# Performance work log

Measured on AMD Instinct MI355X. Metric: run time of the kernel, lower is better.

Reference implementation:

```python
import jax, jax.numpy as jnp
import numpy as np

W, L, D = 4096, 32, 256
WORD_VOCAB, CHR_VOCAB = 50000, 128


def conv1d(x, w, b):
    # x: [N, C_in, T], w: [C_out, C_in, 3], padding=1 (same)
    y = jax.lax.conv_general_dilated(
        x, w, window_strides=(1,), padding=[(1, 1)],
        dimension_numbers=("NCW", "OIW", "NCW"))
    return y + b[None, :, None]


def setup_inputs() -> dict:
    key = jax.random.key(0)
    ks = jax.random.split(key, 12)
    words = jax.random.randint(ks[0], (W,), 0, WORD_VOCAB, dtype=jnp.int32)
    words_in_char = jax.random.randint(ks[1], (W, L), 0, CHR_VOCAB, dtype=jnp.int32)
    s = 0.02
    word_emb = (jax.random.normal(ks[2], (WORD_VOCAB, D), jnp.float32) * s).at[0].set(0.0)  # padding_idx=0
    chr_emb = (jax.random.normal(ks[3], (CHR_VOCAB, D), jnp.float32) * s).at[0].set(0.0)
    conv_chr_w = jax.random.normal(ks[4], (D, D, 3), jnp.float32) * s
    conv_chr_b = jax.random.normal(ks[5], (D,), jnp.float32) * s
    conv_sent_w = jax.random.normal(ks[6], (2 * D, 2 * D, 3), jnp.float32) * s
    conv_sent_b = jax.random.normal(ks[7], (2 * D,), jnp.float32) * s
    w1 = jax.random.normal(ks[8], (4 * D, 2 * D), jnp.float32) * s
    b1 = jax.random.normal(ks[9], (4 * D,), jnp.float32) * s
    w2 = jax.random.normal(ks[10], (2, 4 * D), jnp.float32) * s
    b2 = jax.random.normal(ks[11], (2,), jnp.float32) * s
    return dict(words=words, words_in_char=words_in_char,
                word_emb=word_emb, chr_emb=chr_emb,
                conv_chr_w=conv_chr_w, conv_chr_b=conv_chr_b,
                conv_sent_w=conv_sent_w, conv_sent_b=conv_sent_b,
                w1=w1, b1=b1, w2=w2, b2=b2)


def reference(words, words_in_char, word_emb, chr_emb,
              conv_chr_w, conv_chr_b, conv_sent_w, conv_sent_b,
              w1, b1, w2, b2):
    # word embeddings: [W, D]
    vector_wrds = word_emb[words]
    # char path, batched over all words (equivalent to the per-word loop):
    ch = chr_emb[words_in_char]                      # [W, L, D]
    ch = jnp.transpose(ch, (0, 2, 1))                # [W, D, L]
    wc = conv1d(ch, conv_chr_w, conv_chr_b)          # [W, D, L]
    vector_wchs = jnp.max(wc, axis=2)                # [W, D]
    # sentence conv over the word axis
    u = jnp.concatenate([vector_wrds, vector_wchs], axis=1)  # [W, 2D]
    u = u.T[None, :, :]                              # [1, 2D, W]
    r = conv1d(u, conv_sent_w, conv_sent_b)          # [1, 2D, W]
    r = jnp.max(r, axis=2)                           # [1, 2D]
    h = jnp.tanh(r @ w1.T + b1)                      # [1, 4D]
    return h @ w2.T + b2                             # [1, 2]
```

## Files before the change

kernel.cpp:

```cpp
#include <hip/hip_runtime.h>
#include <hip/hip_bf16.h>
#include <math.h>

#define NW 4096
#define NL 32
#define ND 256
#define ND2 512

typedef __attribute__((ext_vector_type(8))) short short8;
typedef __attribute__((ext_vector_type(4))) float floatx4;

__device__ inline float bfval(short s) {
  union { unsigned u; float f; } v;
  v.u = ((unsigned)(unsigned short)s) << 16;
  return v.f;
}


__global__ __launch_bounds__(256) void prep_kernel(
    const float* __restrict__ conv_sent_w, const float* __restrict__ conv_chr_w,
    float* __restrict__ wT, __hip_bfloat16* __restrict__ Wb,
    short* __restrict__ u_base) {
  int b = blockIdx.x;
  int tid = threadIdx.x;
  if (b < 3072) {
    int idx = b * 256 + tid;
    float v = conv_sent_w[idx];
    int co = idx / 1536;
    int rem = idx - co * 1536;
    int ci = rem / 3;
    int k = rem - ci * 3;
    Wb[k * 262144 + co * 512 + ci] = __float2bfloat16(v);
  } else if (b < 3840) {
    int idx = (b - 3072) * 256 + tid;
    float v = conv_chr_w[idx];
    int co = idx / 768;
    int rem = idx - co * 768;
    int ci = rem / 3;
    int k = rem - ci * 3;
    wT[k * 65536 + ci * 256 + co] = v;
  } else {
    u_base[tid] = 0;
    u_base[tid + 256] = 0;
    u_base[4097 * 512 + tid] = 0;
    u_base[4097 * 512 + tid + 256] = 0;
  }
}

__global__ __launch_bounds__(256) void table_kernel(
    const float* __restrict__ chr_emb, const float* __restrict__ wT,
    __hip_bfloat16* __restrict__ Tb) {
  __shared__ float s_e[4][256];
  int k = blockIdx.x >> 5;
  int c0 = (blockIdx.x & 31) * 4;
  int co = threadIdx.x;
#pragma unroll
  for (int j = 0; j < 4; ++j) s_e[j][co] = chr_emb[(c0 + j) * 256 + co];
  __syncthreads();
  const float* wk = wT + k * 65536;
  float a0 = 0.f, a1 = 0.f, a2 = 0.f, a3 = 0.f;
#pragma unroll 8
  for (int ci = 0; ci < 256; ++ci) {
    float w = wk[ci * 256 + co];
    a0 = fmaf(s_e[0][ci], w, a0);
    a1 = fmaf(s_e[1][ci], w, a1);
    a2 = fmaf(s_e[2][ci], w, a2);
    a3 = fmaf(s_e[3][ci], w, a3);
  }
  int base = ((co >> 6) * 3 + k) * 8192 + (co & 63);
  Tb[base + (c0 + 0) * 64] = __float2bfloat16(a0);
  Tb[base + (c0 + 1) * 64] = __float2bfloat16(a1);
  Tb[base + (c0 + 2) * 64] = __float2bfloat16(a2);
  Tb[base + (c0 + 3) * 64] = __float2bfloat16(a3);
}

__global__ __launch_bounds__(256) void char_word_kernel(
    const int* __restrict__ words, const int* __restrict__ wic,
    const __hip_bfloat16* __restrict__ Tb, const float* __restrict__ word_emb,
    const float* __restrict__ bias, __hip_bfloat16* __restrict__ u0) {
  __shared__ short sT[3 * 128 * 64];
  __shared__ int s_wic[64 * 32];
  __shared__ int s_wid[64];
  int ct = blockIdx.x >> 6;
  int w0 = (blockIdx.x & 63) * 64;
  int tid = threadIdx.x;
  {
    const uint4* src = (const uint4*)((const short*)Tb + ct * 24576);
    uint4* dst = (uint4*)sT;
#pragma unroll
    for (int i = 0; i < 12; ++i) dst[tid + i * 256] = src[tid + i * 256];
    const int4* wsrc = (const int4*)(wic + w0 * 32);
    int4* wdst = (int4*)s_wic;
    wdst[tid] = wsrc[tid];
    wdst[tid + 256] = wsrc[tid + 256];
    if (tid < 64) s_wid[tid] = words[w0 + tid];
  }
  __syncthreads();
  int co_l = tid & 63;
  int slot = tid >> 6;
  float bb = bias[ct * 64 + co_l];
  const short* T0 = sT;
  const short* T1 = sT + 8192;
  const short* T2 = sT + 16384;
  for (int wi = 0; wi < 16; ++wi) {
    int wl = slot * 16 + wi;
    u0[(w0 + wl) * ND2 + ct * 64 + co_l] =
        __float2bfloat16(word_emb[s_wid[wl] * ND + ct * 64 + co_l]);
    const int* ch = s_wic + wl * 32;
    float m = -INFINITY;
#pragma unroll
    for (int t = 0; t < NL; ++t) {
      float s = bfval(T1[ch[t] * 64 + co_l]);
      if (t > 0) s += bfval(T0[ch[t - 1] * 64 + co_l]);
      if (t < NL - 1) s += bfval(T2[ch[t + 1] * 64 + co_l]);
      m = fmaxf(m, s);
    }
    u0[(w0 + wl) * ND2 + ND + ct * 64 + co_l] = __float2bfloat16(m + bb);
  }
}

__global__ __launch_bounds__(256, 2) void sent_conv_mfma(
    const __hip_bfloat16* __restrict__ u0,
    const __hip_bfloat16* __restrict__ Wb,
    float* __restrict__ partial) {
  __shared__ short As[64 * 64];
  __shared__ short Bs[64 * 64];
  __shared__ float sm[4][32];
  const int tid = threadIdx.x;
  const int t0 = blockIdx.x * 64;
  const int co0 = blockIdx.y * 64;
  const int wave = tid >> 6, lane = tid & 63;
  const int wy = wave >> 1, wx = wave & 1;
  const int m = lane & 15, q = lane >> 4;

  floatx4 acc[2][2];
#pragma unroll
  for (int i = 0; i < 2; ++i)
#pragma unroll
    for (int j = 0; j < 2; ++j) acc[i][j] = (floatx4){0.f, 0.f, 0.f, 0.f};

  int aoff[2][2], boff[2][2];
#pragma unroll
  for (int kk = 0; kk < 2; ++kk) {
#pragma unroll
    for (int i = 0; i < 2; ++i) {
      int row = wy * 32 + i * 16 + m;
      aoff[kk][i] = row * 64 + (((kk * 4 + q) ^ (row & 7)) * 8);
      row = wx * 32 + i * 16 + m;
      boff[kk][i] = row * 64 + (((kk * 4 + q) ^ (row & 7)) * 8);
    }
  }

  const int sc = tid & 7, sr = tid >> 3;
  const int swc = (sc ^ (sr & 7)) * 8;
  const short* WbS = (const short*)Wb;
  const short* uS = (const short*)u0;

  for (int s = 0; s < 24; ++s) {
    int k = s >> 3, ci0 = (s & 7) << 6;
    const short* WbK = WbS + k * 262144 + (co0 + sr) * 512 + ci0 + sc * 8;
    const short* uK = uS + (t0 + sr + k - 1) * 512 + ci0 + sc * 8;
    uint4 a0 = *(const uint4*)(WbK);
    uint4 a1 = *(const uint4*)(WbK + 32 * 512);
    uint4 b0 = *(const uint4*)(uK);
    uint4 b1 = *(const uint4*)(uK + 32 * 512);
    *(uint4*)&As[sr * 64 + swc] = a0;
    *(uint4*)&As[(sr + 32) * 64 + swc] = a1;
    *(uint4*)&Bs[sr * 64 + swc] = b0;
    *(uint4*)&Bs[(sr + 32) * 64 + swc] = b1;
    __syncthreads();
#pragma unroll
    for (int kk = 0; kk < 2; ++kk) {
      short8 av0 = *(const short8*)&As[aoff[kk][0]];
      short8 av1 = *(const short8*)&As[aoff[kk][1]];
      short8 bv0 = *(const short8*)&Bs[boff[kk][0]];
      short8 bv1 = *(const short8*)&Bs[boff[kk][1]];
      acc[0][0] = __builtin_amdgcn_mfma_f32_16x16x32_bf16(av0, bv0, acc[0][0], 0, 0, 0);
      acc[0][1] = __builtin_amdgcn_mfma_f32_16x16x32_bf16(av0, bv1, acc[0][1], 0, 0, 0);
      acc[1][0] = __builtin_amdgcn_mfma_f32_16x16x32_bf16(av1, bv0, acc[1][0], 0, 0, 0);
      acc[1][1] = __builtin_amdgcn_mfma_f32_16x16x32_bf16(av1, bv1, acc[1][1], 0, 0, 0);
    }
    __syncthreads();
  }

#pragma unroll
  for (int i = 0; i < 2; ++i)
#pragma unroll
    for (int r = 0; r < 4; ++r) {
      float x = fmaxf(acc[i][0][r], acc[i][1][r]);
#pragma unroll
      for (int off = 1; off < 16; off <<= 1)
        x = fmaxf(x, __shfl_xor(x, off, 64));
      if (m == 0) sm[wave][i * 16 + q * 4 + r] = x;
    }
  __syncthreads();
  if (tid < 64) {
    int whalf = tid >> 5;
    float v = fmaxf(sm[whalf * 2 + 0][tid & 31], sm[whalf * 2 + 1][tid & 31]);
    partial[(co0 + tid) * 64 + blockIdx.x] = v;
  }
}

__global__ __launch_bounds__(512) void fc1_kernel(
    const float* __restrict__ partial, const float* __restrict__ bs,
    const float* __restrict__ w1, const float* __restrict__ b1,
    float* __restrict__ h) {
  __shared__ float s_r[512];
  int tid = threadIdx.x;
  {
    const float4* p = (const float4*)(partial + tid * 64);
    float mm = -INFINITY;
#pragma unroll
    for (int j = 0; j < 16; ++j) {
      float4 v = p[j];
      mm = fmaxf(mm, fmaxf(fmaxf(v.x, v.y), fmaxf(v.z, v.w)));
    }
    s_r[tid] = mm + bs[tid];
  }
  __syncthreads();
  int wave = tid >> 6, lane = tid & 63;
  int o = blockIdx.x * 8 + wave;
  const float4* wv = (const float4*)(w1 + o * 512 + lane * 8);
  const float4* rv = (const float4*)(s_r + lane * 8);
  float4 w0 = wv[0], w1v = wv[1];
  float4 r0 = rv[0], r1 = rv[1];
  float acc = w0.x * r0.x + w0.y * r0.y + w0.z * r0.z + w0.w * r0.w +
              w1v.x * r1.x + w1v.y * r1.y + w1v.z * r1.z + w1v.w * r1.w;
#pragma unroll
  for (int off = 32; off >= 1; off >>= 1) acc += __shfl_down(acc, off, 64);
  if (lane == 0) h[o] = tanhf(acc + b1[o]);
}

__global__ __launch_bounds__(128) void fc2_kernel(
    const float* __restrict__ h, const float* __restrict__ w2,
    const float* __restrict__ b2, float* __restrict__ out) {
  int tid = threadIdx.x;
  int o = tid >> 6;
  int lane = tid & 63;
  float acc = 0.f;
#pragma unroll
  for (int j = 0; j < 16; ++j)
    acc = fmaf(w2[o * 1024 + lane + j * 64], h[lane + j * 64], acc);
#pragma unroll
  for (int off = 32; off >= 1; off >>= 1) acc += __shfl_down(acc, off, 64);
  if (lane == 0) out[o] = acc + b2[o];
}

extern "C" void kernel_launch(void* const* d_in, const int* in_sizes, int n_in,
                              void* d_out, int out_size, void* d_ws, size_t ws_size,
                              hipStream_t stream) {
  const int*   words       = (const int*)d_in[0];
  const int*   wic         = (const int*)d_in[1];
  const float* word_emb    = (const float*)d_in[2];
  const float* chr_emb     = (const float*)d_in[3];
  const float* conv_chr_w  = (const float*)d_in[4];
  const float* conv_chr_b  = (const float*)d_in[5];
  const float* conv_sent_w = (const float*)d_in[6];
  const float* conv_sent_b = (const float*)d_in[7];
  const float* w1          = (const float*)d_in[8];
  const float* b1          = (const float*)d_in[9];
  const float* w2          = (const float*)d_in[10];
  const float* b2          = (const float*)d_in[11];
  float* out = (float*)d_out;

  float* ws    = (float*)d_ws;
  float* wT    = ws;
  float* part  = wT + 196608;
  float* h_buf = part + 32768;
  short* Tb    = (short*)(h_buf + 1024);
  short* u_base = Tb + 98304;
  __hip_bfloat16* u0 = (__hip_bfloat16*)(u_base + 512);
  __hip_bfloat16* Wb = (__hip_bfloat16*)(u_base + 4098 * 512);

  prep_kernel<<<3841, 256, 0, stream>>>(conv_sent_w, conv_chr_w, wT, Wb, u_base);
  table_kernel<<<96, 256, 0, stream>>>(chr_emb, wT, (__hip_bfloat16*)Tb);
  char_word_kernel<<<256, 256, 0, stream>>>(words, wic, (const __hip_bfloat16*)Tb,
                                            word_emb, conv_chr_b, u0);
  sent_conv_mfma<<<dim3(64, 8), 256, 0, stream>>>(u0, Wb, part);
  fc1_kernel<<<128, 512, 0, stream>>>(part, conv_sent_b, w1, b1, h_buf);
  fc2_kernel<<<1, 128, 0, stream>>>(h_buf, w2, b2, out);
}
```

Before: 160.1 us.

## Fuse all stages into one persistent kernel with atomic grid barriers

Replaces six launches with a single 256-block persistent kernel whose stages are separated by software grid barriers built on an atomic counter. The char table build now reads conv_chr_w directly through a shared-memory tile instead of a transposed intermediate. The sentence conv tile grows to 128 time steps per block and software-prefetches the next K slice into registers. This removes launch gaps and the wT round trip, but relies on all 256 blocks being co-resident and adds barrier spin costs plus a memset per call.

New measurement: 241.3 us. 50.7% more time.

```diff
diff --git a/kernel.cpp b/kernel.cpp
--- a/kernel.cpp
+++ b/kernel.cpp
@@ -17,233 +17,266 @@
 }
 
 
-__global__ __launch_bounds__(256) void prep_kernel(
-    const float* __restrict__ conv_sent_w, const float* __restrict__ conv_chr_w,
-    float* __restrict__ wT, __hip_bfloat16* __restrict__ Wb,
-    short* __restrict__ u_base) {
-  int b = blockIdx.x;
-  int tid = threadIdx.x;
-  if (b < 3072) {
-    int idx = b * 256 + tid;
-    float v = conv_sent_w[idx];
-    int co = idx / 1536;
-    int rem = idx - co * 1536;
-    int ci = rem / 3;
-    int k = rem - ci * 3;
-    Wb[k * 262144 + co * 512 + ci] = __float2bfloat16(v);
-  } else if (b < 3840) {
-    int idx = (b - 3072) * 256 + tid;
-    float v = conv_chr_w[idx];
-    int co = idx / 768;
-    int rem = idx - co * 768;
-    int ci = rem / 3;
-    int k = rem - ci * 3;
-    wT[k * 65536 + ci * 256 + co] = v;
+union SMem {
+  struct { float w[256][49]; float e[2][256]; } tab;
+  struct { short T[3 * 128 * 64]; int wic[64 * 32]; int wid[64]; } chr;
+  struct { short As[64 * 64]; short Bs[128 * 64]; float red[4][32]; } sent;
+  struct { float r[512]; } fc;
+};
+
+__device__ __forceinline__ void gbar(int* ctr, int expect) {
+  __syncthreads();
+  if (threadIdx.x == 0) {
+    __hip_atomic_fetch_add(ctr, 1, __ATOMIC_RELEASE, __HIP_MEMORY_SCOPE_AGENT);
+    while (__hip_atomic_load(ctr, __ATOMIC_RELAXED, __HIP_MEMORY_SCOPE_AGENT) < expect)
+      __builtin_amdgcn_s_sleep(8);
+    __builtin_amdgcn_fence(__ATOMIC_ACQUIRE, "agent");
+  }
+  __syncthreads();
+}
+
+__global__ __launch_bounds__(256) void fused_kernel(
+    const int* __restrict__ words, const int* __restrict__ wic,
+    const float* __restrict__ word_emb, const float* __restrict__ chr_emb,
+    const float* __restrict__ conv_chr_w, const float* __restrict__ conv_chr_b,
+    const float* __restrict__ conv_sent_w, const float* __restrict__ conv_sent_b,
+    const float* __restrict__ w1, const float* __restrict__ b1,
+    const float* __restrict__ w2, const float* __restrict__ b2,
+    int* __restrict__ ctr, float* __restrict__ part, float* __restrict__ h_buf,
+    short* __restrict__ Tb, short* __restrict__ u_base,
+    __hip_bfloat16* __restrict__ Wb, float* __restrict__ out) {
+  __shared__ SMem S;
+  const int b = blockIdx.x;
+  const int tid = threadIdx.x;
+
+  if (b >= 64) {
+    int base = (b - 64) * 4096;
+#pragma unroll
+    for (int i = 0; i < 16; ++i) {
+      int idx = base + i * 256 + tid;
+      float v = conv_sent_w[idx];
+      int co = idx / 1536;
+      int rem = idx - co * 1536;
+      int ci = rem / 3;
+      int k = rem - ci * 3;
+      Wb[k * 262144 + co * 512 + ci] = __float2bfloat16(v);
+    }
+    if (b == 255) {
+      u_base[tid] = 0; u_base[tid + 256] = 0;
+      u_base[4097 * 512 + tid] = 0; u_base[4097 * 512 + tid + 256] = 0;
+    }
   } else {
-    u_base[tid] = 0;
-    u_base[tid + 256] = 0;
-    u_base[4097 * 512 + tid] = 0;
-    u_base[4097 * 512 + tid + 256] = 0;
-  }
-}
-
-__global__ __launch_bounds__(256) void table_kernel(
-    const float* __restrict__ chr_emb, const float* __restrict__ wT,
-    __hip_bfloat16* __restrict__ Tb) {
-  __shared__ float s_e[4][256];
-  int k = blockIdx.x >> 5;
-  int c0 = (blockIdx.x & 31) * 4;
-  int co = threadIdx.x;
-#pragma unroll
-  for (int j = 0; j < 4; ++j) s_e[j][co] = chr_emb[(c0 + j) * 256 + co];
-  __syncthreads();
-  const float* wk = wT + k * 65536;
-  float a0 = 0.f, a1 = 0.f, a2 = 0.f, a3 = 0.f;
+    const int c0 = b * 2;
+    const int co = tid;
+    S.tab.e[0][tid] = chr_emb[(c0 + 0) * 256 + tid];
+    S.tab.e[1][tid] = chr_emb[(c0 + 1) * 256 + tid];
+    float acc[2][3] = {};
+    for (int chk = 0; chk < 16; ++chk) {
+      const int ci0 = chk * 16;
+      __syncthreads();
 #pragma unroll 8
-  for (int ci = 0; ci < 256; ++ci) {
-    float w = wk[ci * 256 + co];
-    a0 = fmaf(s_e[0][ci], w, a0);
-    a1 = fmaf(s_e[1][ci], w, a1);
-    a2 = fmaf(s_e[2][ci], w, a2);
-    a3 = fmaf(s_e[3][ci], w, a3);
-  }
-  int base = ((co >> 6) * 3 + k) * 8192 + (co & 63);
-  Tb[base + (c0 + 0) * 64] = __float2bfloat16(a0);
-  Tb[base + (c0 + 1) * 64] = __float2bfloat16(a1);
-  Tb[base + (c0 + 2) * 64] = __float2bfloat16(a2);
-  Tb[base + (c0 + 3) * 64] = __float2bfloat16(a3);
-}
-
-__global__ __launch_bounds__(256) void char_word_kernel(
-    const int* __restrict__ words, const int* __restrict__ wic,
-    const __hip_bfloat16* __restrict__ Tb, const float* __restrict__ word_emb,
-    const float* __restrict__ bias, __hip_bfloat16* __restrict__ u0) {
-  __shared__ short sT[3 * 128 * 64];
-  __shared__ int s_wic[64 * 32];
-  __shared__ int s_wid[64];
-  int ct = blockIdx.x >> 6;
-  int w0 = (blockIdx.x & 63) * 64;
-  int tid = threadIdx.x;
+      for (int i = 0; i < 48; ++i) {
+        int f = tid + i * 256;
+        int wco = f / 48;
+        int j = f - wco * 48;
+        S.tab.w[wco][j] = conv_chr_w[wco * 768 + ci0 * 3 + j];
+      }
+      __syncthreads();
+#pragma unroll
+      for (int ci = 0; ci < 16; ++ci) {
+        float t_w0 = S.tab.w[co][ci * 3 + 0];
+        float t_w1 = S.tab.w[co][ci * 3 + 1];
+        float t_w2 = S.tab.w[co][ci * 3 + 2];
+        float e0 = S.tab.e[0][ci0 + ci];
+        float e1 = S.tab.e[1][ci0 + ci];
+        acc[0][0] = fmaf(e0, t_w0, acc[0][0]);
+        acc[0][1] = fmaf(e0, t_w1, acc[0][1]);
+        acc[0][2] = fmaf(e0, t_w2, acc[0][2]);
+        acc[1][0] = fmaf(e1, t_w0, acc[1][0]);
+        acc[1][1] = fmaf(e1, t_w1, acc[1][1]);
+        acc[1][2] = fmaf(e1, t_w2, acc[1][2]);
+      }
+    }
+    __hip_bfloat16* TbB = (__hip_bfloat16*)Tb;
+    const int tbase = ((co >> 6) * 3) * 8192 + (co & 63);
+#pragma unroll
+    for (int k = 0; k < 3; ++k) {
+      TbB[tbase + k * 8192 + (c0 + 0) * 64] = __float2bfloat16(acc[0][k]);
+      TbB[tbase + k * 8192 + (c0 + 1) * 64] = __float2bfloat16(acc[1][k]);
+    }
+  }
+  gbar(ctr, 256);
+
   {
-    const uint4* src = (const uint4*)((const short*)Tb + ct * 24576);
-    uint4* dst = (uint4*)sT;
+    const int ct = b >> 6;
+    const int w0c = (b & 63) * 64;
+    const uint4* src = (const uint4*)(Tb + ct * 24576);
+    uint4* dst = (uint4*)S.chr.T;
 #pragma unroll
     for (int i = 0; i < 12; ++i) dst[tid + i * 256] = src[tid + i * 256];
-    const int4* wsrc = (const int4*)(wic + w0 * 32);
-    int4* wdst = (int4*)s_wic;
+    const int4* wsrc = (const int4*)(wic + w0c * 32);
+    int4* wdst = (int4*)S.chr.wic;
     wdst[tid] = wsrc[tid];
     wdst[tid + 256] = wsrc[tid + 256];
-    if (tid < 64) s_wid[tid] = words[w0 + tid];
-  }
-  __syncthreads();
-  int co_l = tid & 63;
-  int slot = tid >> 6;
-  float bb = bias[ct * 64 + co_l];
-  const short* T0 = sT;
-  const short* T1 = sT + 8192;
-  const short* T2 = sT + 16384;
-  for (int wi = 0; wi < 16; ++wi) {
-    int wl = slot * 16 + wi;
-    u0[(w0 + wl) * ND2 + ct * 64 + co_l] =
-        __float2bfloat16(word_emb[s_wid[wl] * ND + ct * 64 + co_l]);
-    const int* ch = s_wic + wl * 32;
-    float m = -INFINITY;
-#pragma unroll
-    for (int t = 0; t < NL; ++t) {
-      float s = bfval(T1[ch[t] * 64 + co_l]);
-      if (t > 0) s += bfval(T0[ch[t - 1] * 64 + co_l]);
-      if (t < NL - 1) s += bfval(T2[ch[t + 1] * 64 + co_l]);
-      m = fmaxf(m, s);
-    }
-    u0[(w0 + wl) * ND2 + ND + ct * 64 + co_l] = __float2bfloat16(m + bb);
-  }
-}
-
-__global__ __launch_bounds__(256, 2) void sent_conv_mfma(
-    const __hip_bfloat16* __restrict__ u0,
-    const __hip_bfloat16* __restrict__ Wb,
-    float* __restrict__ partial) {
-  __shared__ short As[64 * 64];
-  __shared__ short Bs[64 * 64];
-  __shared__ float sm[4][32];
-  const int tid = threadIdx.x;
-  const int t0 = blockIdx.x * 64;
-  const int co0 = blockIdx.y * 64;
-  const int wave = tid >> 6, lane = tid & 63;
-  const int wy = wave >> 1, wx = wave & 1;
-  const int m = lane & 15, q = lane >> 4;
-
-  floatx4 acc[2][2];
-#pragma unroll
-  for (int i = 0; i < 2; ++i)
-#pragma unroll
-    for (int j = 0; j < 2; ++j) acc[i][j] = (floatx4){0.f, 0.f, 0.f, 0.f};
-
-  int aoff[2][2], boff[2][2];
-#pragma unroll
-  for (int kk = 0; kk < 2; ++kk) {
-#pragma unroll
-    for (int i = 0; i < 2; ++i) {
-      int row = wy * 32 + i * 16 + m;
-      aoff[kk][i] = row * 64 + (((kk * 4 + q) ^ (row & 7)) * 8);
-      row = wx * 32 + i * 16 + m;
-      boff[kk][i] = row * 64 + (((kk * 4 + q) ^ (row & 7)) * 8);
-    }
-  }
-
-  const int sc = tid & 7, sr = tid >> 3;
-  const int swc = (sc ^ (sr & 7)) * 8;
-  const short* WbS = (const short*)Wb;
-  const short* uS = (const short*)u0;
-
-  for (int s = 0; s < 24; ++s) {
-    int k = s >> 3, ci0 = (s & 7) << 6;
-    const short* WbK = WbS + k * 262144 + (co0 + sr) * 512 + ci0 + sc * 8;
-    const short* uK = uS + (t0 + sr + k - 1) * 512 + ci0 + sc * 8;
-    uint4 a0 = *(const uint4*)(WbK);
-    uint4 a1 = *(const uint4*)(WbK + 32 * 512);
-    uint4 b0 = *(const uint4*)(uK);
-    uint4 b1 = *(const uint4*)(uK + 32 * 512);
-    *(uint4*)&As[sr * 64 + swc] = a0;
-    *(uint4*)&As[(sr + 32) * 64 + swc] = a1;
-    *(uint4*)&Bs[sr * 64 + swc] = b0;
-    *(uint4*)&Bs[(sr + 32) * 64 + swc] = b1;
+    if (tid < 64) S.chr.wid[tid] = words[w0c + tid];
     __syncthreads();
+    const int co_l = tid & 63;
+    const int slot = tid >> 6;
+    const float bb = conv_chr_b[ct * 64 + co_l];
+    const short* T0p = S.chr.T;
+    const short* T1p = S.chr.T + 8192;
+    const short* T2p = S.chr.T + 16384;
+    __hip_bfloat16* u0 = (__hip_bfloat16*)(u_base + 512);
+    for (int wi = 0; wi < 16; ++wi) {
+      int wl = slot * 16 + wi;
+      u0[(w0c + wl) * ND2 + ct * 64 + co_l] =
+          __float2bfloat16(word_emb[S.chr.wid[wl] * ND + ct * 64 + co_l]);
+      const int* ch = S.chr.wic + wl * 32;
+      float mx = -INFINITY;
+#pragma unroll
+      for (int t = 0; t < NL; ++t) {
+        float sv = bfval(T1p[ch[t] * 64 + co_l]);
+        if (t > 0) sv += bfval(T0p[ch[t - 1] * 64 + co_l]);
+        if (t < NL - 1) sv += bfval(T2p[ch[t + 1] * 64 + co_l]);
+        mx = fmaxf(mx, sv);
+      }
+      u0[(w0c + wl) * ND2 + ND + ct * 64 + co_l] = __float2bfloat16(mx + bb);
+    }
+  }
+  gbar(ctr, 512);
+
+  {
+    const int co0 = (b & 7) * 64;
+    const int T0 = (b >> 3) * 128;
+    const int wave = tid >> 6, lane = tid & 63;
+    const int wy = wave >> 1, wx = wave & 1;
+    const int m = lane & 15, q = lane >> 4;
+    floatx4 acc[2][4];
+#pragma unroll
+    for (int i = 0; i < 2; ++i)
+#pragma unroll
+      for (int j = 0; j < 4; ++j) acc[i][j] = (floatx4){0.f, 0.f, 0.f, 0.f};
+
+    int aoff[2][2], boff[2][4];
 #pragma unroll
     for (int kk = 0; kk < 2; ++kk) {
-      short8 av0 = *(const short8*)&As[aoff[kk][0]];
-      short8 av1 = *(const short8*)&As[aoff[kk][1]];
-      short8 bv0 = *(const short8*)&Bs[boff[kk][0]];
-      short8 bv1 = *(const short8*)&Bs[boff[kk][1]];
-      acc[0][0] = __builtin_amdgcn_mfma_f32_16x16x32_bf16(av0, bv0, acc[0][0], 0, 0, 0);
-      acc[0][1] = __builtin_amdgcn_mfma_f32_16x16x32_bf16(av0, bv1, acc[0][1], 0, 0, 0);
-      acc[1][0] = __builtin_amdgcn_mfma_f32_16x16x32_bf16(av1, bv0, acc[1][0], 0, 0, 0);
-      acc[1][1] = __builtin_amdgcn_mfma_f32_16x16x32_bf16(av1, bv1, acc[1][1], 0, 0, 0);
-    }
+#pragma unroll
+      for (int i = 0; i < 2; ++i) {
+        int row = wy * 32 + i * 16 + m;
+        aoff[kk][i] = row * 64 + (((kk * 4 + q) ^ (row & 7)) * 8);
+      }
+#pragma unroll
+      for (int j = 0; j < 4; ++j) {
+        int row = (j >> 1) * 64 + wx * 32 + (j & 1) * 16 + m;
+        boff[kk][j] = row * 64 + (((kk * 4 + q) ^ (row & 7)) * 8);
+      }
+    }
+    const int sc = tid & 7, sr = tid >> 3;
+    const int swc = (sc ^ (sr & 7)) * 8;
+    const short* WbS = (const short*)Wb;
+    const short* uS = u_base + 512;
+
+    uint4 ra0, ra1, rb0, rb1, rb2, rb3;
+    auto LOADS = [&](int s2) {
+      int k = s2 >> 3, ci0 = (s2 & 7) << 6;
+      const short* WbK = WbS + k * 262144 + (co0 + sr) * 512 + ci0 + sc * 8;
+      const short* uK = uS + (T0 + sr + k - 1) * 512 + ci0 + sc * 8;
+      ra0 = *(const uint4*)(WbK);
+      ra1 = *(const uint4*)(WbK + 32 * 512);
+      rb0 = *(const uint4*)(uK);
+      rb1 = *(const uint4*)(uK + 32 * 512);
+      rb2 = *(const uint4*)(uK + 64 * 512);
+      rb3 = *(const uint4*)(uK + 96 * 512);
+    };
+    LOADS(0);
+    for (int s = 0; s < 24; ++s) {
+      *(uint4*)&S.sent.As[sr * 64 + swc] = ra0;
+      *(uint4*)&S.sent.As[(sr + 32) * 64 + swc] = ra1;
+      *(uint4*)&S.sent.Bs[sr * 64 + swc] = rb0;
+      *(uint4*)&S.sent.Bs[(sr + 32) * 64 + swc] = rb1;
+      *(uint4*)&S.sent.Bs[(sr + 64) * 64 + swc] = rb2;
+      *(uint4*)&S.sent.Bs[(sr + 96) * 64 + swc] = rb3;
+      __syncthreads();
+      if (s < 23) LOADS(s + 1);
+#pragma unroll
+      for (int kk = 0; kk < 2; ++kk) {
+        short8 av0 = *(const short8*)&S.sent.As[aoff[kk][0]];
+        short8 av1 = *(const short8*)&S.sent.As[aoff[kk][1]];
+        short8 bv0 = *(const short8*)&S.sent.Bs[boff[kk][0]];
+        short8 bv1 = *(const short8*)&S.sent.Bs[boff[kk][1]];
+        short8 bv2 = *(const short8*)&S.sent.Bs[boff[kk][2]];
+        short8 bv3 = *(const short8*)&S.sent.Bs[boff[kk][3]];
+        acc[0][0] = __builtin_amdgcn_mfma_f32_16x16x32_bf16(av0, bv0, acc[0][0], 0, 0, 0);
+        acc[0][1] = __builtin_amdgcn_mfma_f32_16x16x32_bf16(av0, bv1, acc[0][1], 0, 0, 0);
+        acc[0][2] = __builtin_amdgcn_mfma_f32_16x16x32_bf16(av0, bv2, acc[0][2], 0, 0, 0);
+        acc[0][3] = __builtin_amdgcn_mfma_f32_16x16x32_bf16(av0, bv3, acc[0][3], 0, 0, 0);
+        acc[1][0] = __builtin_amdgcn_mfma_f32_16x16x32_bf16(av1, bv0, acc[1][0], 0, 0, 0);
+        acc[1][1] = __builtin_amdgcn_mfma_f32_16x16x32_bf16(av1, bv1, acc[1][1], 0, 0, 0);
+        acc[1][2] = __builtin_amdgcn_mfma_f32_16x16x32_bf16(av1, bv2, acc[1][2], 0, 0, 0);
+        acc[1][3] = __builtin_amdgcn_mfma_f32_16x16x32_bf16(av1, bv3, acc[1][3], 0, 0, 0);
+      }
+      __syncthreads();
+    }
+#pragma unroll
+    for (int i = 0; i < 2; ++i)
+#pragma unroll
+      for (int r = 0; r < 4; ++r) {
+        float x = fmaxf(fmaxf(acc[i][0][r], acc[i][1][r]),
+                        fmaxf(acc[i][2][r], acc[i][3][r]));
+#pragma unroll
+        for (int off = 1; off < 16; off <<= 1)
+          x = fmaxf(x, __shfl_xor(x, off, 64));
+        if (m == 0) S.sent.red[wave][i * 16 + q * 4 + r] = x;
+      }
     __syncthreads();
-  }
-
-#pragma unroll
-  for (int i = 0; i < 2; ++i)
-#pragma unroll
-    for (int r = 0; r < 4; ++r) {
-      float x = fmaxf(acc[i][0][r], acc[i][1][r]);
-#pragma unroll
-      for (int off = 1; off < 16; off <<= 1)
-        x = fmaxf(x, __shfl_xor(x, off, 64));
-      if (m == 0) sm[wave][i * 16 + q * 4 + r] = x;
-    }
-  __syncthreads();
-  if (tid < 64) {
-    int whalf = tid >> 5;
-    float v = fmaxf(sm[whalf * 2 + 0][tid & 31], sm[whalf * 2 + 1][tid & 31]);
-    partial[(co0 + tid) * 64 + blockIdx.x] = v;
-  }
-}
-
-__global__ __launch_bounds__(512) void fc1_kernel(
-    const float* __restrict__ partial, const float* __restrict__ bs,
-    const float* __restrict__ w1, const float* __restrict__ b1,
-    float* __restrict__ h) {
-  __shared__ float s_r[512];
-  int tid = threadIdx.x;
+    if (tid < 64) {
+      int whalf = tid >> 5;
+      float v = fmaxf(S.sent.red[whalf * 2 + 0][tid & 31],
+                      S.sent.red[whalf * 2 + 1][tid & 31]);
+      part[(co0 + tid) * 32 + (b >> 3)] = v;
+    }
+  }
+  gbar(ctr, 768);
+
   {
-    const float4* p = (const float4*)(partial + tid * 64);
-    float mm = -INFINITY;
-#pragma unroll
-    for (int j = 0; j < 16; ++j) {
-      float4 v = p[j];
-      mm = fmaxf(mm, fmaxf(fmaxf(v.x, v.y), fmaxf(v.z, v.w)));
-    }
-    s_r[tid] = mm + bs[tid];
-  }
-  __syncthreads();
-  int wave = tid >> 6, lane = tid & 63;
-  int o = blockIdx.x * 8 + wave;
-  const float4* wv = (const float4*)(w1 + o * 512 + lane * 8);
-  const float4* rv = (const float4*)(s_r + lane * 8);
-  float4 w0 = wv[0], w1v = wv[1];
-  float4 r0 = rv[0], r1 = rv[1];
-  float acc = w0.x * r0.x + w0.y * r0.y + w0.z * r0.z + w0.w * r0.w +
-              w1v.x * r1.x + w1v.y * r1.y + w1v.z * r1.z + w1v.w * r1.w;
-#pragma unroll
-  for (int off = 32; off >= 1; off >>= 1) acc += __shfl_down(acc, off, 64);
-  if (lane == 0) h[o] = tanhf(acc + b1[o]);
-}
-
-__global__ __launch_bounds__(128) void fc2_kernel(
-    const float* __restrict__ h, const float* __restrict__ w2,
-    const float* __restrict__ b2, float* __restrict__ out) {
-  int tid = threadIdx.x;
-  int o = tid >> 6;
-  int lane = tid & 63;
-  float acc = 0.f;
-#pragma unroll
-  for (int j = 0; j < 16; ++j)
-    acc = fmaf(w2[o * 1024 + lane + j * 64], h[lane + j * 64], acc);
-#pragma unroll
-  for (int off = 32; off >= 1; off >>= 1) acc += __shfl_down(acc, off, 64);
-  if (lane == 0) out[o] = acc + b2[o];
+#pragma unroll
+    for (int rep = 0; rep < 2; ++rep) {
+      int row = tid + rep * 256;
+      const float4* p = (const float4*)(part + row * 32);
+      float mm = -INFINITY;
+#pragma unroll
+      for (int j = 0; j < 8; ++j) {
+        float4 v = p[j];
+        mm = fmaxf(mm, fmaxf(fmaxf(v.x, v.y), fmaxf(v.z, v.w)));
+      }
+      S.fc.r[row] = mm + conv_sent_b[row];
+    }
+    __syncthreads();
+    const int wave = tid >> 6, lane = tid & 63;
+    const int o = b * 4 + wave;
+    const float4* wv = (const float4*)(w1 + o * 512 + lane * 8);
+    const float4* rv = (const float4*)(S.fc.r + lane * 8);
+    float4 wv0 = wv[0], wv1 = wv[1];
+    float4 rv0 = rv[0], rv1 = rv[1];
+    float acc = wv0.x * rv0.x + wv0.y * rv0.y + wv0.z * rv0.z + wv0.w * rv0.w +
+                wv1.x * rv1.x + wv1.y * rv1.y + wv1.z * rv1.z + wv1.w * rv1.w;
+#pragma unroll
+    for (int off = 32; off >= 1; off >>= 1) acc += __shfl_down(acc, off, 64);
+    if (lane == 0) h_buf[o] = tanhf(acc + b1[o]);
+  }
+  gbar(ctr, 1024);
+
+  if (b == 0 && tid < 128) {
+    const int o = tid >> 6;
+    const int lane = tid & 63;
+    float acc2 = 0.f;
+#pragma unroll
+    for (int j = 0; j < 16; ++j)
+      acc2 = fmaf(w2[o * 1024 + lane + j * 64], h_buf[lane + j * 64], acc2);
+#pragma unroll
+    for (int off = 32; off >= 1; off >>= 1) acc2 += __shfl_down(acc2, off, 64);
+    if (lane == 0) out[o] = acc2 + b2[o];
+  }
 }
 
 extern "C" void kernel_launch(void* const* d_in, const int* in_sizes, int n_in,
@@ -264,19 +297,15 @@
   float* out = (float*)d_out;
 
   float* ws    = (float*)d_ws;
-  float* wT    = ws;
-  float* part  = wT + 196608;
-  float* h_buf = part + 32768;
+  int*   ctr   = (int*)ws;
+  float* part  = ws + 4;
+  float* h_buf = part + 16384;
   short* Tb    = (short*)(h_buf + 1024);
   short* u_base = Tb + 98304;
-  __hip_bfloat16* u0 = (__hip_bfloat16*)(u_base + 512);
   __hip_bfloat16* Wb = (__hip_bfloat16*)(u_base + 4098 * 512);
 
-  prep_kernel<<<3841, 256, 0, stream>>>(conv_sent_w, conv_chr_w, wT, Wb, u_base);
-  table_kernel<<<96, 256, 0, stream>>>(chr_emb, wT, (__hip_bfloat16*)Tb);
-  char_word_kernel<<<256, 256, 0, stream>>>(words, wic, (const __hip_bfloat16*)Tb,
-                                            word_emb, conv_chr_b, u0);
-  sent_conv_mfma<<<dim3(64, 8), 256, 0, stream>>>(u0, Wb, part);
-  fc1_kernel<<<128, 512, 0, stream>>>(part, conv_sent_b, w1, b1, h_buf);
-  fc2_kernel<<<1, 128, 0, stream>>>(h_buf, w2, b2, out);
+  hipMemsetAsync(ctr, 0, 16, stream);
+  fused_kernel<<<256, 256, 0, stream>>>(words, wic, word_emb, chr_emb,
+      conv_chr_w, conv_chr_b, conv_sent_w, conv_sent_b, w1, b1, w2, b2,
+      ctr, part, h_buf, Tb, u_base, Wb, out);
 }
```

## Fuse char-weight transpose into table kernel and vectorize char conv gather

Applied to the files above, without the earlier changes.

Merges the prep and table kernels so the char conv table is computed directly from conv_chr_w, staged through shared memory. This removes one launch and the intermediate transposed weight buffer. The char_word kernel now runs twice as many blocks, each handling 32 words, and each lane reads packed bf16 pairs with characters preloaded into registers. The goals are higher occupancy, fewer LDS reads and one less kernel boundary. In exchange, the table part now uses only 64 blocks with a long serial loop, and the larger register array may raise register pressure.

After: 184.7 us. +15.4%, slower.

```diff
diff --git a/kernel.cpp b/kernel.cpp
--- a/kernel.cpp
+++ b/kernel.cpp
@@ -10,68 +10,73 @@
 typedef __attribute__((ext_vector_type(8))) short short8;
 typedef __attribute__((ext_vector_type(4))) float floatx4;
 
-__device__ inline float bfval(short s) {
+__device__ inline float bitsf(unsigned u) {
   union { unsigned u; float f; } v;
-  v.u = ((unsigned)(unsigned short)s) << 16;
+  v.u = u;
   return v.f;
 }
 
 
-__global__ __launch_bounds__(256) void prep_kernel(
+__global__ __launch_bounds__(256) void prep_table_kernel(
     const float* __restrict__ conv_sent_w, const float* __restrict__ conv_chr_w,
-    float* __restrict__ wT, __hip_bfloat16* __restrict__ Wb,
-    short* __restrict__ u_base) {
-  int b = blockIdx.x;
-  int tid = threadIdx.x;
-  if (b < 3072) {
-    int idx = b * 256 + tid;
-    float v = conv_sent_w[idx];
-    int co = idx / 1536;
-    int rem = idx - co * 1536;
-    int ci = rem / 3;
-    int k = rem - ci * 3;
-    Wb[k * 262144 + co * 512 + ci] = __float2bfloat16(v);
-  } else if (b < 3840) {
-    int idx = (b - 3072) * 256 + tid;
-    float v = conv_chr_w[idx];
-    int co = idx / 768;
-    int rem = idx - co * 768;
-    int ci = rem / 3;
-    int k = rem - ci * 3;
-    wT[k * 65536 + ci * 256 + co] = v;
-  } else {
-    u_base[tid] = 0;
-    u_base[tid + 256] = 0;
-    u_base[4097 * 512 + tid] = 0;
-    u_base[4097 * 512 + tid + 256] = 0;
-  }
-}
-
-__global__ __launch_bounds__(256) void table_kernel(
-    const float* __restrict__ chr_emb, const float* __restrict__ wT,
-    __hip_bfloat16* __restrict__ Tb) {
-  __shared__ float s_e[4][256];
-  int k = blockIdx.x >> 5;
-  int c0 = (blockIdx.x & 31) * 4;
-  int co = threadIdx.x;
-#pragma unroll
-  for (int j = 0; j < 4; ++j) s_e[j][co] = chr_emb[(c0 + j) * 256 + co];
-  __syncthreads();
-  const float* wk = wT + k * 65536;
-  float a0 = 0.f, a1 = 0.f, a2 = 0.f, a3 = 0.f;
+    const float* __restrict__ chr_emb, __hip_bfloat16* __restrict__ Wb,
+    __hip_bfloat16* __restrict__ Tb, short* __restrict__ u_base) {
+  __shared__ float s_w[256][49];
+  __shared__ float s_e[2][256];
+  const int b = blockIdx.x;
+  const int tid = threadIdx.x;
+  if (b >= 64) {
+    if (b < 3136) {
+      int idx = (b - 64) * 256 + tid;
+      float v = conv_sent_w[idx];
+      int co = idx / 1536;
+      int rem = idx - co * 1536;
+      int ci = rem / 3;
+      int k = rem - ci * 3;
+      Wb[k * 262144 + co * 512 + ci] = __float2bfloat16(v);
+    } else {
+      u_base[tid] = 0; u_base[tid + 256] = 0;
+      u_base[4097 * 512 + tid] = 0; u_base[4097 * 512 + tid + 256] = 0;
+    }
+    return;
+  }
+  const int c0 = b * 2;
+  const int co = tid;
+  s_e[0][tid] = chr_emb[(c0 + 0) * 256 + tid];
+  s_e[1][tid] = chr_emb[(c0 + 1) * 256 + tid];
+  float acc[2][3] = {};
+  for (int chk = 0; chk < 16; ++chk) {
+    const int ci0 = chk * 16;
+    __syncthreads();
 #pragma unroll 8
-  for (int ci = 0; ci < 256; ++ci) {
-    float w = wk[ci * 256 + co];
-    a0 = fmaf(s_e[0][ci], w, a0);
-    a1 = fmaf(s_e[1][ci], w, a1);
-    a2 = fmaf(s_e[2][ci], w, a2);
-    a3 = fmaf(s_e[3][ci], w, a3);
-  }
-  int base = ((co >> 6) * 3 + k) * 8192 + (co & 63);
-  Tb[base + (c0 + 0) * 64] = __float2bfloat16(a0);
-  Tb[base + (c0 + 1) * 64] = __float2bfloat16(a1);
-  Tb[base + (c0 + 2) * 64] = __float2bfloat16(a2);
-  Tb[base + (c0 + 3) * 64] = __float2bfloat16(a3);
+    for (int i = 0; i < 48; ++i) {
+      int f = tid + i * 256;
+      int wco = f / 48;
+      int j = f - wco * 48;
+      s_w[wco][j] = conv_chr_w[wco * 768 + ci0 * 3 + j];
+    }
+    __syncthreads();
+#pragma unroll
+    for (int ci = 0; ci < 16; ++ci) {
+      float t_w0 = s_w[co][ci * 3 + 0];
+      float t_w1 = s_w[co][ci * 3 + 1];
+      float t_w2 = s_w[co][ci * 3 + 2];
+      float e0 = s_e[0][ci0 + ci];
+      float e1 = s_e[1][ci0 + ci];
+      acc[0][0] = fmaf(e0, t_w0, acc[0][0]);
+      acc[0][1] = fmaf(e0, t_w1, acc[0][1]);
+      acc[0][2] = fmaf(e0, t_w2, acc[0][2]);
+      acc[1][0] = fmaf(e1, t_w0, acc[1][0]);
+      acc[1][1] = fmaf(e1, t_w1, acc[1][1]);
+      acc[1][2] = fmaf(e1, t_w2, acc[1][2]);
+    }
+  }
+  const int tbase = ((co >> 6) * 3) * 8192 + (co & 63);
+#pragma unroll
+  for (int k = 0; k < 3; ++k) {
+    Tb[tbase + k * 8192 + (c0 + 0) * 64] = __float2bfloat16(acc[0][k]);
+    Tb[tbase + k * 8192 + (c0 + 1) * 64] = __float2bfloat16(acc[1][k]);
+  }
 }
 
 __global__ __launch_bounds__(256) void char_word_kernel(
@@ -79,43 +84,69 @@
     const __hip_bfloat16* __restrict__ Tb, const float* __restrict__ word_emb,
     const float* __restrict__ bias, __hip_bfloat16* __restrict__ u0) {
   __shared__ short sT[3 * 128 * 64];
-  __shared__ int s_wic[64 * 32];
-  __shared__ int s_wid[64];
-  int ct = blockIdx.x >> 6;
-  int w0 = (blockIdx.x & 63) * 64;
-  int tid = threadIdx.x;
+  __shared__ int s_wic[32 * 32];
+  __shared__ int s_wid[32];
+  const int ct = blockIdx.x >> 7;
+  const int w0 = (blockIdx.x & 127) * 32;
+  const int tid = threadIdx.x;
   {
     const uint4* src = (const uint4*)((const short*)Tb + ct * 24576);
     uint4* dst = (uint4*)sT;
 #pragma unroll
     for (int i = 0; i < 12; ++i) dst[tid + i * 256] = src[tid + i * 256];
-    const int4* wsrc = (const int4*)(wic + w0 * 32);
-    int4* wdst = (int4*)s_wic;
-    wdst[tid] = wsrc[tid];
-    wdst[tid + 256] = wsrc[tid + 256];
-    if (tid < 64) s_wid[tid] = words[w0 + tid];
+    ((int4*)s_wic)[tid] = ((const int4*)(wic + w0 * 32))[tid];
+    if (tid < 32) s_wid[tid] = words[w0 + tid];
   }
   __syncthreads();
-  int co_l = tid & 63;
-  int slot = tid >> 6;
-  float bb = bias[ct * 64 + co_l];
-  const short* T0 = sT;
-  const short* T1 = sT + 8192;
-  const short* T2 = sT + 16384;
-  for (int wi = 0; wi < 16; ++wi) {
-    int wl = slot * 16 + wi;
-    u0[(w0 + wl) * ND2 + ct * 64 + co_l] =
-        __float2bfloat16(word_emb[s_wid[wl] * ND + ct * 64 + co_l]);
-    const int* ch = s_wic + wl * 32;
-    float m = -INFINITY;
+  {
+    const int co_l = tid & 63, slot = tid >> 6;
+#pragma unroll
+    for (int wi = 0; wi < 8; ++wi) {
+      int wl = slot * 8 + wi;
+      u0[(w0 + wl) * ND2 + ct * 64 + co_l] =
+          __float2bfloat16(word_emb[s_wid[wl] * ND + ct * 64 + co_l]);
+    }
+  }
+  const int wave = tid >> 6, lane = tid & 63;
+  const int half = lane >> 5, co2 = (lane & 31) * 2;
+  const float2 bb = *(const float2*)&bias[ct * 64 + co2];
+  const short* T0p = sT;
+  const short* T1p = sT + 8192;
+  const short* T2p = sT + 16384;
+#pragma unroll
+  for (int p = 0; p < 4; ++p) {
+    const int wl = wave * 8 + p * 2 + half;
+    int chv[32];
+    const int4* c4 = (const int4*)(s_wic + wl * 32);
+#pragma unroll
+    for (int j = 0; j < 8; ++j) {
+      int4 cc = c4[j];
+      chv[4 * j + 0] = cc.x; chv[4 * j + 1] = cc.y;
+      chv[4 * j + 2] = cc.z; chv[4 * j + 3] = cc.w;
+    }
+    float m0 = -INFINITY, m1 = -INFINITY;
 #pragma unroll
     for (int t = 0; t < NL; ++t) {
-      float s = bfval(T1[ch[t] * 64 + co_l]);
-      if (t > 0) s += bfval(T0[ch[t - 1] * 64 + co_l]);
-      if (t < NL - 1) s += bfval(T2[ch[t + 1] * 64 + co_l]);
-      m = fmaxf(m, s);
-    }
-    u0[(w0 + wl) * ND2 + ND + ct * 64 + co_l] = __float2bfloat16(m + bb);
+      unsigned v1 = *(const unsigned*)&T1p[chv[t] * 64 + co2];
+      float s0 = bitsf(v1 << 16);
+      float s1 = bitsf(v1 & 0xffff0000u);
+      if (t > 0) {
+        unsigned v0 = *(const unsigned*)&T0p[chv[t - 1] * 64 + co2];
+        s0 += bitsf(v0 << 16);
+        s1 += bitsf(v0 & 0xffff0000u);
+      }
+      if (t < NL - 1) {
+        unsigned v2 = *(const unsigned*)&T2p[chv[t + 1] * 64 + co2];
+        s0 += bitsf(v2 << 16);
+        s1 += bitsf(v2 & 0xffff0000u);
+      }
+      m0 = fmaxf(m0, s0);
+      m1 = fmaxf(m1, s1);
+    }
+    __hip_bfloat162 hh;
+    hh.x = __float2bfloat16(m0 + bb.x);
+    hh.y = __float2bfloat16(m1 + bb.y);
+    *(__hip_bfloat162*)&u0[(w0 + wl) * ND2 + ND + ct * 64 + co2] = hh;
   }
 }
 
@@ -264,17 +295,16 @@
   float* out = (float*)d_out;
 
   float* ws    = (float*)d_ws;
-  float* wT    = ws;
-  float* part  = wT + 196608;
+  float* part  = ws;
   float* h_buf = part + 32768;
   short* Tb    = (short*)(h_buf + 1024);
   short* u_base = Tb + 98304;
   __hip_bfloat16* u0 = (__hip_bfloat16*)(u_base + 512);
   __hip_bfloat16* Wb = (__hip_bfloat16*)(u_base + 4098 * 512);
 
-  prep_kernel<<<3841, 256, 0, stream>>>(conv_sent_w, conv_chr_w, wT, Wb, u_base);
-  table_kernel<<<96, 256, 0, stream>>>(chr_emb, wT, (__hip_bfloat16*)Tb);
-  char_word_kernel<<<256, 256, 0, stream>>>(words, wic, (const __hip_bfloat16*)Tb,
+  prep_table_kernel<<<3137, 256, 0, stream>>>(conv_sent_w, conv_chr_w, chr_emb,
+                                              Wb, (__hip_bfloat16*)Tb, u_base);
+  char_word_kernel<<<512, 256, 0, stream>>>(words, wic, (const __hip_bfloat16*)Tb,
                                             word_emb, conv_chr_b, u0);
   sent_conv_mfma<<<dim3(64, 8), 256, 0, stream>>>(u0, Wb, part);
   fc1_kernel<<<128, 512, 0, stream>>>(part, conv_sent_b, w1, b1, h_buf);
```
